# Kernel optimization log

Hardware: AMD Instinct MI355X
Metric: run time of the kernel (lower is better)

The kernel has to match this reference:

```python
import jax, jax.numpy as jnp
import numpy as np

EPS = 1e-5
N, K, CIN, COUT = 100000, 27, 64, 128


def sparse_conv(x, nbr, W):
    # x: [N, C]; nbr: [N, K] with sentinel index N meaning 'no neighbor'
    x_pad = jnp.concatenate([x, jnp.zeros((1, x.shape[1]), x.dtype)], axis=0)  # [N+1, C]
    g = x_pad[nbr]  # gather: [N, K, C]
    return jnp.einsum('nkc,kcd->nd', g, W)  # per-offset GEMM, scatter to output sites


def bn_relu(y, gamma, beta):
    # BatchNorm over active sites (training-mode batch statistics), then ReLU
    mu = y.mean(axis=0)
    var = y.var(axis=0)
    return jax.nn.relu((y - mu) * jax.lax.rsqrt(var + EPS) * gamma + beta)


def setup_inputs() -> dict:
    key = jax.random.key(0)
    ks = jax.random.split(key, 5)
    x = jax.random.normal(ks[0], (N, CIN), dtype=jnp.float32)
    # sentinel N indicates missing neighbor (maps to zero-padded row)
    nbr = jax.random.randint(ks[1], (N, K), 0, N + 1)
    W1 = jax.random.normal(ks[2], (K, CIN, COUT), dtype=jnp.float32) * (1.0 / np.sqrt(K * CIN))
    W2 = jax.random.normal(ks[3], (K, COUT, COUT), dtype=jnp.float32) * (1.0 / np.sqrt(K * COUT))
    W_skip = jax.random.normal(ks[4], (CIN, COUT), dtype=jnp.float32) * (1.0 / np.sqrt(CIN))
    return {
        'x': x, 'nbr': nbr,
        'W1': W1, 'gamma1': jnp.ones((COUT,), jnp.float32), 'beta1': jnp.zeros((COUT,), jnp.float32),
        'W2': W2, 'gamma2': jnp.ones((COUT,), jnp.float32), 'beta2': jnp.zeros((COUT,), jnp.float32),
        'W_skip': W_skip,
    }


def reference(x, nbr, W1, gamma1, beta1, W2, gamma2, beta2, W_skip):
    identity = x @ W_skip                      # 1x1 conv skip (same coords)
    h = bn_relu(sparse_conv(x, nbr, W1), gamma1, beta1)
    h = bn_relu(sparse_conv(h, nbr, W2), gamma2, beta2)
    return h + identity
```

## Files before the change

### kernel.cpp

```cpp
#include <hip/hip_runtime.h>
#include <hip/hip_bf16.h>

#define NSITES 100000
#define KOFFS 27
#define CIN 64
#define COUT 128

typedef unsigned short u16;
typedef __attribute__((ext_vector_type(8))) short s16x8;
typedef __attribute__((ext_vector_type(4))) float f32x4;

static __device__ __forceinline__ u16 f2bf(float f) {
    union { float f; unsigned u; } x; x.f = f;
    return (u16)((x.u + 0x7FFFu + ((x.u >> 16) & 1u)) >> 16);
}
static __device__ __forceinline__ float bf2f(u16 v) {
    union { unsigned u; float f; } x; x.u = ((unsigned)v) << 16;
    return x.f;
}

static __device__ __forceinline__ void lds_barrier() {
    asm volatile("s_waitcnt lgkmcnt(0)" ::: "memory");
    __builtin_amdgcn_s_barrier();
    __builtin_amdgcn_sched_barrier(0);
}

__global__ void prep_kernel(const float* __restrict__ W1, const float* __restrict__ W2,
                            const float* __restrict__ Wsk,
                            u16* __restrict__ W1t, u16* __restrict__ W2t,
                            u16* __restrict__ Wskt, float* __restrict__ zero_area) {
    int i = blockIdx.x * 256 + threadIdx.x;
    if (i < 27 * 64 * 128) {
        int k = i / 8192, r = i & 8191, d = r >> 6, c = r & 63;
        W1t[i] = f2bf(W1[k * 8192 + c * 128 + d]);
        return;
    }
    i -= 27 * 64 * 128;
    if (i < 27 * 128 * 128) {
        int k = i / 16384, r = i & 16383, d = r >> 7, c = r & 127;
        W2t[i] = f2bf(W2[k * 16384 + c * 128 + d]);
        return;
    }
    i -= 27 * 128 * 128;
    if (i < 8192) {
        int d = i >> 6, c = i & 63;
        Wskt[i] = f2bf(Wsk[c * 128 + d]);
        return;
    }
    i -= 8192;
    zero_area[i] = 0.0f;
}

__global__ void convert_x_kernel(const float* __restrict__ x, u16* __restrict__ xb) {
    long long e = ((long long)blockIdx.x * 256 + threadIdx.x) * 8;
    if (e >= (long long)(NSITES + 1) * CIN) return;
    s16x8 o;
    if (e < (long long)NSITES * CIN) {
        float4 v0 = *(const float4*)(x + e);
        float4 v1 = *(const float4*)(x + e + 4);
        o[0] = (short)f2bf(v0.x); o[1] = (short)f2bf(v0.y);
        o[2] = (short)f2bf(v0.z); o[3] = (short)f2bf(v0.w);
        o[4] = (short)f2bf(v1.x); o[5] = (short)f2bf(v1.y);
        o[6] = (short)f2bf(v1.z); o[7] = (short)f2bf(v1.w);
    } else {
#pragma unroll
        for (int j = 0; j < 8; ++j) o[j] = 0;
    }
    *(s16x8*)(xb + e) = o;
}

template <int CK, bool IDENT_FUSE, bool STATS>
__global__ __launch_bounds__(256, 4) void conv_kernel(
    const u16* __restrict__ xin, const int* __restrict__ nbr,
    const u16* __restrict__ Wt, u16* __restrict__ yout,
    float* __restrict__ psum, float* __restrict__ psq, int nk,
    const u16* __restrict__ Wskt, float* __restrict__ outid) {
    constexpr int STRIDE = CK + 4;
    constexpr int KSTEPS = CK / 32;
    constexpr int CPR = CK / 8;
    constexpr int RPP = 256 / CPR;
    constexpr int NPASS = 64 / RPP;
    __shared__ __align__(16) u16 a_tile[2][64 * STRIDE];
    __shared__ int nbr_tile[64 * KOFFS];

    const int tid = threadIdx.x;
    const int wave = tid >> 6;
    const int lane = tid & 63;
    const int m = lane & 15;
    const int q = lane >> 4;
    const int n0 = blockIdx.x * 64;
    const int wc = wave * 32;
    const int srow = tid / CPR;
    const int schunk = tid % CPR;

    for (int i = tid; i < 64 * KOFFS; i += 256) {
        int r = i / KOFFS;
        int kk = i - r * KOFFS;
        int row = n0 + r;
        nbr_tile[i] = (row < NSITES) ? nbr[row * KOFFS + kk] : NSITES;
    }
    __syncthreads();

    f32x4 acc[4][2];
#pragma unroll
    for (int rt = 0; rt < 4; ++rt)
#pragma unroll
        for (int ct = 0; ct < 2; ++ct)
#pragma unroll
            for (int r = 0; r < 4; ++r) acc[rt][ct][r] = 0.0f;

    s16x8 ag0[NPASS], ag1[NPASS];
#pragma unroll
    for (int p = 0; p < NPASS; ++p) {
        int r = p * RPP + srow;
        ag0[p] = *(const s16x8*)(xin + (long long)nbr_tile[r * KOFFS] * CK + schunk * 8);
    }
    if (nk > 1) {
#pragma unroll
        for (int p = 0; p < NPASS; ++p) {
            int r = p * RPP + srow;
            ag1[p] = *(const s16x8*)(xin + (long long)nbr_tile[r * KOFFS + 1] * CK + schunk * 8);
        }
    }
#pragma unroll
    for (int p = 0; p < NPASS; ++p)
        *(s16x8*)(&a_tile[0][(p * RPP + srow) * STRIDE + schunk * 8]) = ag0[p];
    if (nk > 2) {
#pragma unroll
        for (int p = 0; p < NPASS; ++p) {
            int r = p * RPP + srow;
            ag0[p] = *(const s16x8*)(xin + (long long)nbr_tile[r * KOFFS + 2] * CK + schunk * 8);
        }
    }
    lds_barrier();

    auto conv_iter = [&](int k, s16x8 (&wset)[NPASS]) {
        s16x8 bf[2][KSTEPS];
        const u16* wb = Wt + (long long)k * (COUT * CK);
#pragma unroll
        for (int ct = 0; ct < 2; ++ct)
#pragma unroll
            for (int ks = 0; ks < KSTEPS; ++ks)
                bf[ct][ks] = *(const s16x8*)(wb + (wc + ct * 16 + m) * CK + ks * 32 + q * 8);

        const int cur = k & 1;
        if (k + 1 < nk) {
#pragma unroll
            for (int p = 0; p < NPASS; ++p)
                *(s16x8*)(&a_tile[cur ^ 1][(p * RPP + srow) * STRIDE + schunk * 8]) = wset[p];
            if (k + 3 < nk) {
#pragma unroll
                for (int p = 0; p < NPASS; ++p) {
                    int r = p * RPP + srow;
                    wset[p] = *(const s16x8*)(xin + (long long)nbr_tile[r * KOFFS + k + 3] * CK + schunk * 8);
                }
            }
        }

#pragma unroll
        for (int ks = 0; ks < KSTEPS; ++ks) {
            s16x8 af[4];
#pragma unroll
            for (int rt = 0; rt < 4; ++rt)
                af[rt] = *(const s16x8*)(&a_tile[cur][(rt * 16 + m) * STRIDE + ks * 32 + q * 8]);
#pragma unroll
            for (int rt = 0; rt < 4; ++rt)
#pragma unroll
                for (int ct = 0; ct < 2; ++ct)
                    acc[rt][ct] = __builtin_amdgcn_mfma_f32_16x16x32_bf16(
                        af[rt], bf[ct][ks], acc[rt][ct], 0, 0, 0);
        }
        lds_barrier();
    };

    int k = 0;
    for (; k + 1 < nk; k += 2) {
        conv_iter(k, ag1);
        conv_iter(k + 1, ag0);
    }
    if (k < nk) conv_iter(k, ag1);

#pragma unroll
    for (int rt = 0; rt < 4; ++rt) {
        int rowb = n0 + rt * 16 + q * 4;
#pragma unroll
        for (int ct = 0; ct < 2; ++ct) {
            int col = wc + ct * 16 + m;
#pragma unroll
            for (int r = 0; r < 4; ++r) {
                int row = rowb + r;
                if (row < NSITES) yout[(long long)row * COUT + col] = f2bf(acc[rt][ct][r]);
            }
        }
    }

    if (STATS) {
#pragma unroll
        for (int ct = 0; ct < 2; ++ct) {
            float s = 0.f, ss = 0.f;
#pragma unroll
            for (int rt = 0; rt < 4; ++rt)
#pragma unroll
                for (int r = 0; r < 4; ++r) {
                    float v = acc[rt][ct][r];
                    s += v; ss += v * v;
                }
            s += __shfl_xor(s, 16); ss += __shfl_xor(ss, 16);
            s += __shfl_xor(s, 32); ss += __shfl_xor(ss, 32);
            if (q == 0) {
                int col = wc + ct * 16 + m;
                int slot = blockIdx.x & 63;
                atomicAdd(psum + slot * COUT + col, s);
                atomicAdd(psq + slot * COUT + col, ss);
            }
        }
    }

    if (IDENT_FUSE) {
#pragma unroll
        for (int rt = 0; rt < 4; ++rt)
#pragma unroll
            for (int ct = 0; ct < 2; ++ct)
#pragma unroll
                for (int r = 0; r < 4; ++r) acc[rt][ct][r] = 0.0f;
        s16x8 aid[NPASS];
#pragma unroll
        for (int p = 0; p < NPASS; ++p) {
            int row = n0 + p * RPP + srow;
            long long idx = (row < NSITES) ? row : NSITES;
            aid[p] = *(const s16x8*)(xin + idx * CK + schunk * 8);
        }
        s16x8 bfi[2][KSTEPS];
#pragma unroll
        for (int ct = 0; ct < 2; ++ct)
#pragma unroll
            for (int ks = 0; ks < KSTEPS; ++ks)
                bfi[ct][ks] = *(const s16x8*)(Wskt + (wc + ct * 16 + m) * CK + ks * 32 + q * 8);
#pragma unroll
        for (int p = 0; p < NPASS; ++p)
            *(s16x8*)(&a_tile[0][(p * RPP + srow) * STRIDE + schunk * 8]) = aid[p];
        lds_barrier();
#pragma unroll
        for (int ks = 0; ks < KSTEPS; ++ks) {
            s16x8 af[4];
#pragma unroll
            for (int rt = 0; rt < 4; ++rt)
                af[rt] = *(const s16x8*)(&a_tile[0][(rt * 16 + m) * STRIDE + ks * 32 + q * 8]);
#pragma unroll
            for (int rt = 0; rt < 4; ++rt)
#pragma unroll
                for (int ct = 0; ct < 2; ++ct)
                    acc[rt][ct] = __builtin_amdgcn_mfma_f32_16x16x32_bf16(
                        af[rt], bfi[ct][ks], acc[rt][ct], 0, 0, 0);
        }
#pragma unroll
        for (int rt = 0; rt < 4; ++rt) {
            int rowb = n0 + rt * 16 + q * 4;
#pragma unroll
            for (int ct = 0; ct < 2; ++ct) {
                int col = wc + ct * 16 + m;
#pragma unroll
                for (int r = 0; r < 4; ++r) {
                    int row = rowb + r;
                    if (row < NSITES) outid[(long long)row * COUT + col] = acc[rt][ct][r];
                }
            }
        }
    }
}

__global__ void bn_stats_kernel(const float* __restrict__ psum, const float* __restrict__ psq,
                                const float* __restrict__ gamma, const float* __restrict__ beta,
                                float* __restrict__ ab) {
    int col = threadIdx.x;
    float s = 0.f, ss = 0.f;
    for (int i = 0; i < 64; ++i) { s += psum[i * COUT + col]; ss += psq[i * COUT + col]; }
    const float inv_n = 1.0f / (float)NSITES;
    float mu = s * inv_n;
    float var = ss * inv_n - mu * mu;
    float rs = rsqrtf(var + 1e-5f);
    float a = gamma[col] * rs;
    ab[col] = a;
    ab[COUT + col] = beta[col] - mu * a;
}

__global__ void bn_apply_kernel(const u16* __restrict__ y, const float* __restrict__ ab,
                                u16* __restrict__ h) {
    long long e = ((long long)blockIdx.x * 256 + threadIdx.x) * 8;
    if (e >= (long long)(NSITES + 1) * COUT) return;
    s16x8 o;
    if (e < (long long)NSITES * COUT) {
        int cb = (int)(e & (COUT - 1));
        s16x8 v = *(const s16x8*)(y + e);
#pragma unroll
        for (int j = 0; j < 8; ++j) {
            float r = bf2f((u16)v[j]) * ab[cb + j] + ab[COUT + cb + j];
            o[j] = (short)f2bf(fmaxf(r, 0.f));
        }
    } else {
#pragma unroll
        for (int j = 0; j < 8; ++j) o[j] = 0;
    }
    *(s16x8*)(h + e) = o;
}

__global__ void final_kernel(const u16* __restrict__ y, const float* __restrict__ ab,
                             float* __restrict__ out) {
    long long e = ((long long)blockIdx.x * 256 + threadIdx.x) * 8;
    if (e >= (long long)NSITES * COUT) return;
    int cb = (int)(e & (COUT - 1));
    s16x8 v = *(const s16x8*)(y + e);
    float4 i0 = *(const float4*)(out + e);
    float4 i1 = *(const float4*)(out + e + 4);
    float is[8] = {i0.x, i0.y, i0.z, i0.w, i1.x, i1.y, i1.z, i1.w};
    float os[8];
#pragma unroll
    for (int j = 0; j < 8; ++j) {
        float r = bf2f((u16)v[j]) * ab[cb + j] + ab[COUT + cb + j];
        os[j] = fmaxf(r, 0.f) + is[j];
    }
    *(float4*)(out + e) = make_float4(os[0], os[1], os[2], os[3]);
    *(float4*)(out + e + 4) = make_float4(os[4], os[5], os[6], os[7]);
}

extern "C" void kernel_launch(void* const* d_in, const int* in_sizes, int n_in,
                              void* d_out, int out_size, void* d_ws, size_t ws_size,
                              hipStream_t stream) {
    const float* x   = (const float*)d_in[0];
    const int*   nbr = (const int*)d_in[1];
    const float* W1  = (const float*)d_in[2];
    const float* g1  = (const float*)d_in[3];
    const float* b1  = (const float*)d_in[4];
    const float* W2  = (const float*)d_in[5];
    const float* g2  = (const float*)d_in[6];
    const float* b2  = (const float*)d_in[7];
    const float* Wsk = (const float*)d_in[8];
    float* out = (float*)d_out;

    char* ws = (char*)d_ws;
    u16*   xb   = (u16*)(ws);
    u16*   W1t  = (u16*)(ws + 12800128);
    u16*   W2t  = (u16*)(ws + 13242496);
    u16*   Wskt = (u16*)(ws + 14127232);
    u16*   y    = (u16*)(ws + 14143616);
    u16*   h1   = (u16*)(ws + 39743616);
    float* ps1  = (float*)(ws + 65343872);
    float* pq1  = ps1 + 8192;
    float* ps2  = pq1 + 8192;
    float* pq2  = ps2 + 8192;
    float* ab1  = pq2 + 8192;
    float* ab2  = ab1 + 256;

    const int NBLK = (NSITES + 63) / 64;

    prep_kernel<<<2752, 256, 0, stream>>>(W1, W2, Wsk, W1t, W2t, Wskt, ps1);
    convert_x_kernel<<<3126, 256, 0, stream>>>(x, xb);
    conv_kernel<64, true, true><<<NBLK, 256, 0, stream>>>(xb, nbr, W1t, y, ps1, pq1, KOFFS, Wskt, out);
    bn_stats_kernel<<<1, 128, 0, stream>>>(ps1, pq1, g1, b1, ab1);
    bn_apply_kernel<<<6251, 256, 0, stream>>>(y, ab1, h1);
    conv_kernel<128, false, true><<<NBLK, 256, 0, stream>>>(h1, nbr, W2t, y, ps2, pq2, KOFFS, nullptr, nullptr);
    bn_stats_kernel<<<1, 128, 0, stream>>>(ps2, pq2, g2, b2, ab2);
    final_kernel<<<6250, 256, 0, stream>>>(y, ab2, out);
}
```

Baseline: 460.1 us.

## Add dedicated producer wave using direct global-to-LDS gathers with 4-stage ring

```diff
diff --git a/kernel.cpp b/kernel.cpp
--- a/kernel.cpp
+++ b/kernel.cpp
@@ -23,6 +23,12 @@
     asm volatile("s_waitcnt lgkmcnt(0)" ::: "memory");
     __builtin_amdgcn_s_barrier();
     __builtin_amdgcn_sched_barrier(0);
+}
+
+static __device__ __forceinline__ void gld_lds16(const u16* src, u16* dst) {
+    __builtin_amdgcn_global_load_lds((const __attribute__((address_space(1))) void*)src,
+                                     (__attribute__((address_space(3))) void*)dst,
+                                     16, 0, 0);
 }
 
 __global__ void prep_kernel(const float* __restrict__ W1, const float* __restrict__ W2,
@@ -70,17 +76,17 @@
 }
 
 template <int CK, bool IDENT_FUSE, bool STATS>
-__global__ __launch_bounds__(256, 4) void conv_kernel(
+__global__ __launch_bounds__(320, 4) void conv_kernel(
     const u16* __restrict__ xin, const int* __restrict__ nbr,
     const u16* __restrict__ Wt, u16* __restrict__ yout,
     float* __restrict__ psum, float* __restrict__ psq, int nk,
     const u16* __restrict__ Wskt, float* __restrict__ outid) {
-    constexpr int STRIDE = CK + 4;
     constexpr int KSTEPS = CK / 32;
     constexpr int CPR = CK / 8;
-    constexpr int RPP = 256 / CPR;
-    constexpr int NPASS = 64 / RPP;
-    __shared__ __align__(16) u16 a_tile[2][64 * STRIDE];
+    constexpr int SET_ELEMS = 64 * CK;
+    constexpr int GLD_PER_SET = (64 * CK * 2) / 1024;
+    constexpr int RPI = 1024 / (CK * 2);
+    __shared__ __align__(16) u16 a_tile[4 * SET_ELEMS];
     __shared__ int nbr_tile[64 * KOFFS];
 
     const int tid = threadIdx.x;
@@ -90,10 +96,8 @@
     const int q = lane >> 4;
     const int n0 = blockIdx.x * 64;
     const int wc = wave * 32;
-    const int srow = tid / CPR;
-    const int schunk = tid % CPR;
-
-    for (int i = tid; i < 64 * KOFFS; i += 256) {
+
+    for (int i = tid; i < 64 * KOFFS; i += 320) {
         int r = i / KOFFS;
         int kk = i - r * KOFFS;
         int row = n0 + r;
@@ -109,150 +113,79 @@
 #pragma unroll
             for (int r = 0; r < 4; ++r) acc[rt][ct][r] = 0.0f;
 
-    s16x8 ag0[NPASS], ag1[NPASS];
-#pragma unroll
-    for (int p = 0; p < NPASS; ++p) {
-        int r = p * RPP + srow;
-        ag0[p] = *(const s16x8*)(xin + (long long)nbr_tile[r * KOFFS] * CK + schunk * 8);
-    }
-    if (nk > 1) {
-#pragma unroll
-        for (int p = 0; p < NPASS; ++p) {
-            int r = p * RPP + srow;
-            ag1[p] = *(const s16x8*)(xin + (long long)nbr_tile[r * KOFFS + 1] * CK + schunk * 8);
-        }
-    }
-#pragma unroll
-    for (int p = 0; p < NPASS; ++p)
-        *(s16x8*)(&a_tile[0][(p * RPP + srow) * STRIDE + schunk * 8]) = ag0[p];
-    if (nk > 2) {
-#pragma unroll
-        for (int p = 0; p < NPASS; ++p) {
-            int r = p * RPP + srow;
-            ag0[p] = *(const s16x8*)(xin + (long long)nbr_tile[r * KOFFS + 2] * CK + schunk * 8);
+    auto issue_set = [&](int kt) {
+        u16* dst = a_tile + (kt & 3) * SET_ELEMS;
+        const int r_ = lane / CPR;
+        const int c_ = lane % CPR;
+#pragma unroll
+        for (int j = 0; j < GLD_PER_SET; ++j) {
+            int r = j * RPI + r_;
+            int cl = c_ ^ (r & 7);
+            const u16* src = xin + (long long)nbr_tile[r * KOFFS + kt] * CK + cl * 8;
+            gld_lds16(src, dst + j * 512);
+        }
+    };
+
+    if (wave == 4) {
+        issue_set(0);
+        if (nk > 1) issue_set(1);
+        if (nk > 2) issue_set(2);
+        const int younger = ((nk > 1) ? 1 : 0) + ((nk > 2) ? 1 : 0);
+        if constexpr (CK == 128) {
+            if (younger == 2)      asm volatile("s_waitcnt vmcnt(32)" ::: "memory");
+            else if (younger == 1) asm volatile("s_waitcnt vmcnt(16)" ::: "memory");
+            else                   asm volatile("s_waitcnt vmcnt(0)" ::: "memory");
+        } else {
+            if (younger == 2)      asm volatile("s_waitcnt vmcnt(16)" ::: "memory");
+            else if (younger == 1) asm volatile("s_waitcnt vmcnt(8)" ::: "memory");
+            else                   asm volatile("s_waitcnt vmcnt(0)" ::: "memory");
         }
     }
     lds_barrier();
 
-    auto conv_iter = [&](int k, s16x8 (&wset)[NPASS]) {
-        s16x8 bf[2][KSTEPS];
-        const u16* wb = Wt + (long long)k * (COUT * CK);
-#pragma unroll
-        for (int ct = 0; ct < 2; ++ct)
-#pragma unroll
-            for (int ks = 0; ks < KSTEPS; ++ks)
-                bf[ct][ks] = *(const s16x8*)(wb + (wc + ct * 16 + m) * CK + ks * 32 + q * 8);
-
-        const int cur = k & 1;
-        if (k + 1 < nk) {
-#pragma unroll
-            for (int p = 0; p < NPASS; ++p)
-                *(s16x8*)(&a_tile[cur ^ 1][(p * RPP + srow) * STRIDE + schunk * 8]) = wset[p];
-            if (k + 3 < nk) {
-#pragma unroll
-                for (int p = 0; p < NPASS; ++p) {
-                    int r = p * RPP + srow;
-                    wset[p] = *(const s16x8*)(xin + (long long)nbr_tile[r * KOFFS + k + 3] * CK + schunk * 8);
+    for (int k = 0; k < nk; ++k) {
+        if (wave == 4) {
+            if (k + 3 < nk) issue_set(k + 3);
+            if (k + 1 < nk) {
+                const int younger = ((k + 2 < nk) ? 1 : 0) + ((k + 3 < nk) ? 1 : 0);
+                if constexpr (CK == 128) {
+                    if (younger == 2)      asm volatile("s_waitcnt vmcnt(32)" ::: "memory");
+                    else if (younger == 1) asm volatile("s_waitcnt vmcnt(16)" ::: "memory");
+                    else                   asm volatile("s_waitcnt vmcnt(0)" ::: "memory");
+                } else {
+                    if (younger == 2)      asm volatile("s_waitcnt vmcnt(16)" ::: "memory");
+                    else if (younger == 1) asm volatile("s_waitcnt vmcnt(8)" ::: "memory");
+                    else                   asm volatile("s_waitcnt vmcnt(0)" ::: "memory");
                 }
             }
-        }
-
-#pragma unroll
-        for (int ks = 0; ks < KSTEPS; ++ks) {
-            s16x8 af[4];
-#pragma unroll
-            for (int rt = 0; rt < 4; ++rt)
-                af[rt] = *(const s16x8*)(&a_tile[cur][(rt * 16 + m) * STRIDE + ks * 32 + q * 8]);
-#pragma unroll
-            for (int rt = 0; rt < 4; ++rt)
-#pragma unroll
-                for (int ct = 0; ct < 2; ++ct)
-                    acc[rt][ct] = __builtin_amdgcn_mfma_f32_16x16x32_bf16(
-                        af[rt], bf[ct][ks], acc[rt][ct], 0, 0, 0);
+        } else {
+            s16x8 bf[2][KSTEPS];
+            const u16* wb = Wt + (long long)k * (COUT * CK);
+#pragma unroll
+            for (int ct = 0; ct < 2; ++ct)
+#pragma unroll
+                for (int ks = 0; ks < KSTEPS; ++ks)
+                    bf[ct][ks] = *(const s16x8*)(wb + (wc + ct * 16 + m) * CK + ks * 32 + q * 8);
+
+            const u16* aset = a_tile + (k & 3) * SET_ELEMS;
+#pragma unroll
+            for (int ks = 0; ks < KSTEPS; ++ks) {
+                s16x8 af[4];
+#pragma unroll
+                for (int rt = 0; rt < 4; ++rt)
+                    af[rt] = *(const s16x8*)(aset + (rt * 16 + m) * CK + (((ks * 4 + q) ^ (m & 7)) * 8));
+#pragma unroll
+                for (int rt = 0; rt < 4; ++rt)
+#pragma unroll
+                    for (int ct = 0; ct < 2; ++ct)
+                        acc[rt][ct] = __builtin_amdgcn_mfma_f32_16x16x32_bf16(
+                            af[rt], bf[ct][ks], acc[rt][ct], 0, 0, 0);
+            }
         }
         lds_barrier();
-    };
-
-    int k = 0;
-    for (; k + 1 < nk; k += 2) {
-        conv_iter(k, ag1);
-        conv_iter(k + 1, ag0);
-    }
-    if (k < nk) conv_iter(k, ag1);
-
-#pragma unroll
-    for (int rt = 0; rt < 4; ++rt) {
-        int rowb = n0 + rt * 16 + q * 4;
-#pragma unroll
-        for (int ct = 0; ct < 2; ++ct) {
-            int col = wc + ct * 16 + m;
-#pragma unroll
-            for (int r = 0; r < 4; ++r) {
-                int row = rowb + r;
-                if (row < NSITES) yout[(long long)row * COUT + col] = f2bf(acc[rt][ct][r]);
-            }
-        }
-    }
-
-    if (STATS) {
-#pragma unroll
-        for (int ct = 0; ct < 2; ++ct) {
-            float s = 0.f, ss = 0.f;
-#pragma unroll
-            for (int rt = 0; rt < 4; ++rt)
-#pragma unroll
-                for (int r = 0; r < 4; ++r) {
-                    float v = acc[rt][ct][r];
-                    s += v; ss += v * v;
-                }
-            s += __shfl_xor(s, 16); ss += __shfl_xor(ss, 16);
-            s += __shfl_xor(s, 32); ss += __shfl_xor(ss, 32);
-            if (q == 0) {
-                int col = wc + ct * 16 + m;
-                int slot = blockIdx.x & 63;
-                atomicAdd(psum + slot * COUT + col, s);
-                atomicAdd(psq + slot * COUT + col, ss);
-            }
-        }
-    }
-
-    if (IDENT_FUSE) {
-#pragma unroll
-        for (int rt = 0; rt < 4; ++rt)
-#pragma unroll
-            for (int ct = 0; ct < 2; ++ct)
-#pragma unroll
-                for (int r = 0; r < 4; ++r) acc[rt][ct][r] = 0.0f;
-        s16x8 aid[NPASS];
-#pragma unroll
-        for (int p = 0; p < NPASS; ++p) {
-            int row = n0 + p * RPP + srow;
-            long long idx = (row < NSITES) ? row : NSITES;
-            aid[p] = *(const s16x8*)(xin + idx * CK + schunk * 8);
-        }
-        s16x8 bfi[2][KSTEPS];
-#pragma unroll
-        for (int ct = 0; ct < 2; ++ct)
-#pragma unroll
-            for (int ks = 0; ks < KSTEPS; ++ks)
-                bfi[ct][ks] = *(const s16x8*)(Wskt + (wc + ct * 16 + m) * CK + ks * 32 + q * 8);
-#pragma unroll
-        for (int p = 0; p < NPASS; ++p)
-            *(s16x8*)(&a_tile[0][(p * RPP + srow) * STRIDE + schunk * 8]) = aid[p];
-        lds_barrier();
-#pragma unroll
-        for (int ks = 0; ks < KSTEPS; ++ks) {
-            s16x8 af[4];
-#pragma unroll
-            for (int rt = 0; rt < 4; ++rt)
-                af[rt] = *(const s16x8*)(&a_tile[0][(rt * 16 + m) * STRIDE + ks * 32 + q * 8]);
-#pragma unroll
-            for (int rt = 0; rt < 4; ++rt)
-#pragma unroll
-                for (int ct = 0; ct < 2; ++ct)
-                    acc[rt][ct] = __builtin_amdgcn_mfma_f32_16x16x32_bf16(
-                        af[rt], bfi[ct][ks], acc[rt][ct], 0, 0, 0);
-        }
+    }
+
+    if (wave < 4) {
 #pragma unroll
         for (int rt = 0; rt < 4; ++rt) {
             int rowb = n0 + rt * 16 + q * 4;
@@ -262,7 +195,80 @@
 #pragma unroll
                 for (int r = 0; r < 4; ++r) {
                     int row = rowb + r;
-                    if (row < NSITES) outid[(long long)row * COUT + col] = acc[rt][ct][r];
+                    if (row < NSITES) yout[(long long)row * COUT + col] = f2bf(acc[rt][ct][r]);
+                }
+            }
+        }
+
+        if (STATS) {
+#pragma unroll
+            for (int ct = 0; ct < 2; ++ct) {
+                float s = 0.f, ss = 0.f;
+#pragma unroll
+                for (int rt = 0; rt < 4; ++rt)
+#pragma unroll
+                    for (int r = 0; r < 4; ++r) {
+                        float v = acc[rt][ct][r];
+                        s += v; ss += v * v;
+                    }
+                s += __shfl_xor(s, 16); ss += __shfl_xor(ss, 16);
+                s += __shfl_xor(s, 32); ss += __shfl_xor(ss, 32);
+                if (q == 0) {
+                    int col = wc + ct * 16 + m;
+                    int slot = blockIdx.x & 63;
+                    atomicAdd(psum + slot * COUT + col, s);
+                    atomicAdd(psq + slot * COUT + col, ss);
+                }
+            }
+        }
+    }
+
+    if (IDENT_FUSE) {
+        for (int idx = tid; idx < 64 * CPR; idx += 320) {
+            int r = idx / CPR, c = idx - r * CPR;
+            int row = n0 + r;
+            long long gidx = (row < NSITES) ? row : NSITES;
+            s16x8 v = *(const s16x8*)(xin + gidx * CK + c * 8);
+            *(s16x8*)(a_tile + r * CK + ((c ^ (r & 7)) * 8)) = v;
+        }
+        lds_barrier();
+        if (wave < 4) {
+#pragma unroll
+            for (int rt = 0; rt < 4; ++rt)
+#pragma unroll
+                for (int ct = 0; ct < 2; ++ct)
+#pragma unroll
+                    for (int r = 0; r < 4; ++r) acc[rt][ct][r] = 0.0f;
+            s16x8 bfi[2][KSTEPS];
+#pragma unroll
+            for (int ct = 0; ct < 2; ++ct)
+#pragma unroll
+                for (int ks = 0; ks < KSTEPS; ++ks)
+                    bfi[ct][ks] = *(const s16x8*)(Wskt + (wc + ct * 16 + m) * CK + ks * 32 + q * 8);
+#pragma unroll
+            for (int ks = 0; ks < KSTEPS; ++ks) {
+                s16x8 af[4];
+#pragma unroll
+                for (int rt = 0; rt < 4; ++rt)
+                    af[rt] = *(const s16x8*)(a_tile + (rt * 16 + m) * CK + (((ks * 4 + q) ^ (m & 7)) * 8));
+#pragma unroll
+                for (int rt = 0; rt < 4; ++rt)
+#pragma unroll
+                    for (int ct = 0; ct < 2; ++ct)
+                        acc[rt][ct] = __builtin_amdgcn_mfma_f32_16x16x32_bf16(
+                            af[rt], bfi[ct][ks], acc[rt][ct], 0, 0, 0);
+            }
+#pragma unroll
+            for (int rt = 0; rt < 4; ++rt) {
+                int rowb = n0 + rt * 16 + q * 4;
+#pragma unroll
+                for (int ct = 0; ct < 2; ++ct) {
+                    int col = wc + ct * 16 + m;
+#pragma unroll
+                    for (int r = 0; r < 4; ++r) {
+                        int row = rowb + r;
+                        if (row < NSITES) outid[(long long)row * COUT + col] = acc[rt][ct][r];
+                    }
                 }
             }
         }
@@ -355,10 +361,10 @@
 
     prep_kernel<<<2752, 256, 0, stream>>>(W1, W2, Wsk, W1t, W2t, Wskt, ps1);
     convert_x_kernel<<<3126, 256, 0, stream>>>(x, xb);
-    conv_kernel<64, true, true><<<NBLK, 256, 0, stream>>>(xb, nbr, W1t, y, ps1, pq1, KOFFS, Wskt, out);
+    conv_kernel<64, true, true><<<NBLK, 320, 0, stream>>>(xb, nbr, W1t, y, ps1, pq1, KOFFS, Wskt, out);
     bn_stats_kernel<<<1, 128, 0, stream>>>(ps1, pq1, g1, b1, ab1);
     bn_apply_kernel<<<6251, 256, 0, stream>>>(y, ab1, h1);
-    conv_kernel<128, false, true><<<NBLK, 256, 0, stream>>>(h1, nbr, W2t, y, ps2, pq2, KOFFS, nullptr, nullptr);
+    conv_kernel<128, false, true><<<NBLK, 320, 0, stream>>>(h1, nbr, W2t, y, ps2, pq2, KOFFS, nullptr, nullptr);
     bn_stats_kernel<<<1, 128, 0, stream>>>(ps2, pq2, g2, b2, ab2);
     final_kernel<<<6250, 256, 0, stream>>>(y, ab2, out);
 }
```

Result: slower. 568.4 us (+23.5%).
